# Kernel optimization log

Measured on AMD Instinct MI355X. Metric: run time of the kernel, lower is better.

Reference implementation:

```python
import jax, jax.numpy as jnp
import numpy as np
from functools import reduce

N = 20          # total qubits
N_SQC = 4       # shadow-circuit qubits
REPEAT = 2      # BasicEntangleLayer repeat
CDTYPE = jnp.complex64

_I2 = jnp.eye(2, dtype=CDTYPE)
_X  = jnp.array([[0, 1], [1, 0]], dtype=CDTYPE)   # PauliX
_P0 = jnp.array([[1, 0], [0, 0]], dtype=CDTYPE)
_P1 = jnp.array([[0, 0], [0, 1]], dtype=CDTYPE)


def multi_kron(mats):
    return reduce(jnp.kron, mats)


def _ry(t):
    c = jnp.cos(t * 0.5).astype(CDTYPE)
    s = jnp.sin(t * 0.5).astype(CDTYPE)
    return jnp.stack([jnp.stack([c, -s]), jnp.stack([s, c])])


def _rz(t):
    e = jnp.exp(-0.5j * t.astype(CDTYPE))
    z = jnp.zeros((), CDTYPE)
    return jnp.stack([jnp.stack([e, z]), jnp.stack([z, jnp.conj(e)])])


def _yzy_layer(p, n):
    # per qubit i: Ry(p[3i]) then Rz(p[3i+1]) then Ry(p[3i+2])
    mats = [_ry(p[3 * i + 2]) @ _rz(p[3 * i + 1]) @ _ry(p[3 * i]) for i in range(n)]
    return multi_kron(mats)


def _cnot(c, t, n):
    a = [_I2] * n; a[c] = _P0
    b = [_I2] * n; b[c] = _P1; b[t] = _X
    return multi_kron(a) + multi_kron(b)


def _ring_of_cnot(n):
    U = jnp.eye(2 ** n, dtype=CDTYPE)
    for i in range(n):
        U = _cnot(i, (i + 1) % n, n) @ U
    return U


def build_circuit(weight):
    """BasicEntangleLayer (YZY rotations + ring of CNOTs, repeated) + final YZYLayer."""
    n = N_SQC
    ring = _ring_of_cnot(n)
    U = jnp.eye(2 ** n, dtype=CDTYPE)
    for r in range(REPEAT):
        p = weight[3 * n * r:3 * n * (r + 1)]
        U = ring @ (_yzy_layer(p, n) @ U)
    U = _yzy_layer(weight[3 * n * REPEAT:3 * n * (REPEAT + 1)], n) @ U
    return U


def setup_inputs() -> dict:
    key = jax.random.key(0)
    k1, k2 = jax.random.split(key)
    vector_batch = jax.random.normal(k1, (32, 2 ** N), dtype=jnp.float32)
    weight = jax.random.uniform(k2, (9 * N_SQC,), dtype=jnp.float32,
                                minval=0.0, maxval=2.0 * np.pi)
    return {"vector_batch": vector_batch, "weight": weight}


def reference(vector_batch, weight):
    B = vector_batch.shape[0]
    # row-wise L2 normalization, then amplitude encoding into 2^N complex state
    norm = jnp.linalg.norm(vector_batch, axis=1, keepdims=True)
    state = (vector_batch / jnp.maximum(norm, 1e-12)).astype(CDTYPE)  # (B, 2^N)

    U = build_circuit(weight)                        # (16, 16)
    M = multi_kron([_X] * N_SQC)                     # X^{\otimes n_sqc}
    temp = U.conj().T @ M @ U                        # (16, 16) Hermitian

    d = 2 ** N_SQC
    outs = []
    for q in range(N - N_SQC + 1):
        # apply temp locally on qubits [q, q+n_sqc): identical math to
        # <state| I^{\otimes q} (x) temp (x) I^{\otimes rest} |state>
        s = state.reshape(B, 2 ** q, d, -1)          # (B, left, 16, right)
        ts = jnp.einsum('ij,bajc->baic', temp, s)
        outs.append(jnp.einsum('bajc,bajc->b', s.conj(), ts).real)
    return jnp.stack(outs, axis=1).astype(jnp.float32)  # (B, N-n_sqc+1)
```

## Files before the change

### kernel.cpp

```cpp
#include <hip/hip_runtime.h>
#include <math.h>

#define WS_TU    0
#define WS_S     256
#define WS_N     800
#define WS_PART  1024
#define WS_NPART 35840
#define WS_NEED_BYTES ((WS_NPART + 2048) * 4)

typedef _Float16 half8 __attribute__((ext_vector_type(8)));
typedef float f32x4 __attribute__((ext_vector_type(4)));

__device__ inline float2 cmul2(float2 a, float2 b) {
  return make_float2(a.x * b.x - a.y * b.y, a.x * b.y + a.y * b.x);
}

__device__ inline int ringperm(int x) {
  if ((x >> 3) & 1) x ^= 4;
  if ((x >> 2) & 1) x ^= 2;
  if ((x >> 1) & 1) x ^= 1;
  if (x & 1)        x ^= 8;
  return x;
}

__device__ inline float2 yzy_elem(const float* wgt, int layer, int r, int c) {
  float2 prod = make_float2(1.f, 0.f);
#pragma unroll
  for (int k = 0; k < 4; k++) {
    float t0 = wgt[layer * 12 + 3 * k + 0];
    float t1 = wgt[layer * 12 + 3 * k + 1];
    float t2 = wgt[layer * 12 + 3 * k + 2];
    float s0, c0, s1, c1, s2, c2;
    sincosf(0.5f * t0, &s0, &c0);
    sincosf(0.5f * t1, &s1, &c1);
    sincosf(0.5f * t2, &s2, &c2);
    float A = c2 * c0, B = s2 * s0, C = c2 * s0, D = s2 * c0;
    float2 m00 = make_float2( c1 * (A - B), -s1 * (A + B));
    float2 m01 = make_float2(-c1 * (C + D),  s1 * (C - D));
    float2 m10 = make_float2( c1 * (C + D),  s1 * (C - D));
    float2 m11 = make_float2( c1 * (A - B),  s1 * (A + B));
    int rb = (r >> (3 - k)) & 1, cb = (c >> (3 - k)) & 1;
    float2 mm = rb ? (cb ? m11 : m10) : (cb ? m01 : m00);
    prod = cmul2(prod, mm);
  }
  return prod;
}

__global__ void build_T_kernel(const float* __restrict__ wgt, float* __restrict__ ws) {
  __shared__ float2 U[256], Y[256], W[256];
  const int t = threadIdx.x;
  const int r = t >> 4, c = t & 15;

  U[t] = yzy_elem(wgt, 0, r, c);
  __syncthreads();
  W[ringperm(r) * 16 + c] = U[t];
  __syncthreads(); U[t] = W[t]; __syncthreads();
  Y[t] = yzy_elem(wgt, 1, r, c);
  __syncthreads();
  {
    float2 s = make_float2(0.f, 0.f);
#pragma unroll
    for (int k = 0; k < 16; k++) {
      float2 pr = cmul2(Y[r * 16 + k], U[k * 16 + c]);
      s.x += pr.x; s.y += pr.y;
    }
    W[t] = s;
  }
  __syncthreads(); U[t] = W[t]; __syncthreads();
  W[ringperm(r) * 16 + c] = U[t];
  __syncthreads(); U[t] = W[t]; __syncthreads();
  Y[t] = yzy_elem(wgt, 2, r, c);
  __syncthreads();
  {
    float2 s = make_float2(0.f, 0.f);
#pragma unroll
    for (int k = 0; k < 16; k++) {
      float2 pr = cmul2(Y[r * 16 + k], U[k * 16 + c]);
      s.x += pr.x; s.y += pr.y;
    }
    W[t] = s;
  }
  __syncthreads(); U[t] = W[t]; __syncthreads();
  Y[t] = U[(r ^ 15) * 16 + c];
  __syncthreads();
  float s_re = 0.f;
#pragma unroll
  for (int k = 0; k < 16; k++) {
    float2 u = U[k * 16 + r], m = Y[k * 16 + c];
    s_re += u.x * m.x + u.y * m.y;
  }
  ws[WS_TU + t] = s_re;
}

__device__ inline int swzB(int B) {
  int h = B >> 3;
  int f = (h ^ (h >> 3) ^ (h >> 6)) & 7;
  return B ^ f;
}

template <int P>
__device__ inline float windowM(const half8* __restrict__ HB, const float* __restrict__ Tr) {
  const int t = threadIdx.x;
  const int w = t >> 6, l = t & 63, g = l >> 4, i = l & 15;
  f32x4 h0 = {0.f, 0.f, 0.f, 0.f}, h1 = {0.f, 0.f, 0.f, 0.f};
#pragma unroll
  for (int s = 0; s < 4; s++) {
    int rest0 = (w << 5) | (s << 2) | g;
    int rest1 = (w << 5) | ((s + 4) << 2) | g;
    int rl0 = rest0 & ((1 << (P - 3)) - 1), rh0 = rest0 >> (P - 3);
    int rl1 = rest1 & ((1 << (P - 3)) - 1), rh1 = rest1 >> (P - 3);
    int pos0 = (rl0 << 3) | (i << P) | (rh0 << (P + 4));
    int pos1 = (rl1 << 3) | (i << P) | (rh1 << (P + 4));
    half8 f0 = HB[swzB(pos0 >> 3)];
    half8 f1 = HB[swzB(pos1 >> 3)];
    h0 = __builtin_amdgcn_mfma_f32_16x16x32_f16(f0, f0, h0, 0, 0, 0);
    h1 = __builtin_amdgcn_mfma_f32_16x16x32_f16(f1, f1, h1, 0, 0, 0);
  }
  float part = 0.f;
#pragma unroll
  for (int reg = 0; reg < 4; reg++) part = fmaf(Tr[reg], h0[reg] + h1[reg], part);
  return part;
}

__global__ __launch_bounds__(256) void passAll_kernel(const float* __restrict__ vb,
                                                      float* ws, int use_part) {
  __shared__ half8 HB[2048];
  const int t = threadIdx.x;
  const int bid = blockIdx.x;

  int mode, idx;
  if (bid < 4096) {
    int gph = bid >> 4, s = bid & 15;
    mode = s >> 3;
    idx = gph * 8 + (s & 7);
  } else {
    mode = 2;
    idx = bid - 4096;
  }
  const int b = idx >> 6, chunk = idx & 63;
  const int l = t & 63, g = l >> 4, i = l & 15;

  float Treg[4];
#pragma unroll
  for (int reg = 0; reg < 4; reg++) Treg[reg] = ws[WS_TU + ((g * 4 + reg) << 4) + i];

  float nsum = 0.f;
  if (mode == 0) {
    const float4* src4 = ((const float4*)vb) + ((size_t)b << 18) + ((size_t)chunk << 12);
#pragma unroll
    for (int j = 0; j < 8; j++) {
      int B = j * 256 + t;
      float4 a = src4[2 * B], c = src4[2 * B + 1];
      nsum = fmaf(a.x, a.x, nsum); nsum = fmaf(a.y, a.y, nsum);
      nsum = fmaf(a.z, a.z, nsum); nsum = fmaf(a.w, a.w, nsum);
      nsum = fmaf(c.x, c.x, nsum); nsum = fmaf(c.y, c.y, nsum);
      nsum = fmaf(c.z, c.z, nsum); nsum = fmaf(c.w, c.w, nsum);
      half8 h;
      h[0] = (_Float16)a.x; h[1] = (_Float16)a.y; h[2] = (_Float16)a.z; h[3] = (_Float16)a.w;
      h[4] = (_Float16)c.x; h[5] = (_Float16)c.y; h[6] = (_Float16)c.z; h[7] = (_Float16)c.w;
      HB[swzB(B)] = h;
    }
  } else if (mode == 1) {
    const float* srcf = vb + ((size_t)b << 20) + ((size_t)chunk << 14);
#pragma unroll
    for (int j = 0; j < 8; j++) {
      int B = j * 256 + t;
      half8 h;
#pragma unroll
      for (int e = 0; e < 8; e++) h[e] = (_Float16)srcf[e * 2048 + B];
      HB[swzB(B)] = h;
    }
  } else {
    const float4* src4 = ((const float4*)vb) + ((size_t)b << 18) + chunk * 8;
#pragma unroll
    for (int j = 0; j < 8; j++) {
      int B = j * 256 + t;
      int row = B >> 2;
      int c4 = (B & 3) * 2;
      float4 a = src4[row * 512 + c4], c = src4[row * 512 + c4 + 1];
      half8 h;
      h[0] = (_Float16)a.x; h[1] = (_Float16)a.y; h[2] = (_Float16)a.z; h[3] = (_Float16)a.w;
      h[4] = (_Float16)c.x; h[5] = (_Float16)c.y; h[6] = (_Float16)c.z; h[7] = (_Float16)c.w;
      HB[swzB(B)] = h;
    }
  }
  __syncthreads();

  float part[8];
#pragma unroll
  for (int k = 0; k < 8; k++) part[k] = 0.f;

  int nwin;
#define DOWIN(P, WIN) part[WIN] = windowM<P>(HB, Treg);
  if (mode == 0) {
    nwin = 8;
    DOWIN(3, 0) DOWIN(4, 1) DOWIN(5, 2) DOWIN(6, 3)
    DOWIN(7, 4) DOWIN(8, 5) DOWIN(9, 6) DOWIN(10, 7)
  } else if (mode == 1) {
    nwin = 3;
    DOWIN(3, 0) DOWIN(4, 1) DOWIN(5, 2)
  } else {
    nwin = 6;
    DOWIN(5, 0) DOWIN(6, 1) DOWIN(7, 2)
    DOWIN(8, 3) DOWIN(9, 4) DOWIN(10, 5)
  }
#undef DOWIN
  __syncthreads();

  float* red2 = (float*)HB;
#pragma unroll
  for (int k = 0; k < 8; k++) red2[k * 256 + t] = part[k];
  red2[8 * 256 + t] = nsum;
  __syncthreads();

  const int win = t >> 5, idx32 = t & 31;
  const float4* r4 = (const float4*)red2;
  float4 q0 = r4[win * 64 + idx32], q1 = r4[win * 64 + 32 + idx32];
  float s1 = (q0.x + q0.y + q0.z + q0.w) + (q1.x + q1.y + q1.z + q1.w);
#pragma unroll
  for (int off = 16; off; off >>= 1) s1 += __shfl_down(s1, off, 32);

  float s2 = 0.f;
  if (mode == 0 && win == 0) {
    float4 n0 = r4[8 * 64 + idx32], n1 = r4[8 * 64 + 32 + idx32];
    s2 = (n0.x + n0.y + n0.z + n0.w) + (n1.x + n1.y + n1.z + n1.w);
#pragma unroll
    for (int off = 16; off; off >>= 1) s2 += __shfl_down(s2, off, 32);
  }

  const int qbase = (mode == 0) ? 13 : (mode == 1) ? 16 : 5;
  if (idx32 == 0 && win < nwin) {
    int q = qbase - win;
    if (use_part) ws[WS_PART + (b * 17 + q) * 64 + chunk] = s1;
    else          atomicAdd(ws + WS_S + b * 17 + q, s1);
  }
  if (mode == 0 && t == 0) {
    if (use_part) ws[WS_NPART + b * 64 + chunk] = s2;
    else          atomicAdd(ws + WS_N + b, s2);
  }
}

__global__ void finalize_kernel(const float* __restrict__ ws, float* __restrict__ out,
                                int use_part) {
  int i = blockIdx.x * 256 + threadIdx.x;
  if (i < 544) {
    int b = i / 17;
    float s, n;
    if (use_part) {
      const float* sp = ws + WS_PART + i * 64;
      s = 0.f;
#pragma unroll 8
      for (int c = 0; c < 64; c++) s += sp[c];
      const float* np = ws + WS_NPART + b * 64;
      n = 0.f;
#pragma unroll 8
      for (int c = 0; c < 64; c++) n += np[c];
    } else {
      s = ws[WS_S + i];
      n = ws[WS_N + b];
    }
    out[i] = s / fmaxf(n, 1e-24f);
  }
}

extern "C" void kernel_launch(void* const* d_in, const int* in_sizes, int n_in,
                              void* d_out, int out_size, void* d_ws, size_t ws_size,
                              hipStream_t stream) {
  const float* vb  = (const float*)d_in[0];
  const float* wgt = (const float*)d_in[1];
  float* out = (float*)d_out;
  float* ws  = (float*)d_ws;
  int use_part = (ws_size >= (size_t)WS_NEED_BYTES) ? 1 : 0;

  hipMemsetAsync(d_ws, 0, 4096, stream);
  build_T_kernel<<<1, 256, 0, stream>>>(wgt, ws);
  passAll_kernel<<<6144, 256, 0, stream>>>(vb, ws, use_part);
  finalize_kernel<<<3, 256, 0, stream>>>(ws, out, use_part);
}
```

Baseline: 68.80 us.

## Fuse high-qubit windows into mode-0 blocks via in-register transpose

Drops the separate mode-1 blocks, which re-read the input with strided scalar loads to build the layout needed for qubit windows 14-16. Mode-0 blocks now keep their converted half8 values in registers, transpose them into shared memory after the first eight windows, and evaluate those three windows themselves. This removes one third of the blocks and their global reads. The cost is longer mode-0 blocks with extra register pressure, two more barriers, and a reworked reduction over twelve 16-lane groups.

```diff
diff --git a/kernel.cpp b/kernel.cpp
--- a/kernel.cpp
+++ b/kernel.cpp
@@ -128,15 +128,8 @@
   const int t = threadIdx.x;
   const int bid = blockIdx.x;
 
-  int mode, idx;
-  if (bid < 4096) {
-    int gph = bid >> 4, s = bid & 15;
-    mode = s >> 3;
-    idx = gph * 8 + (s & 7);
-  } else {
-    mode = 2;
-    idx = bid - 4096;
-  }
+  const int mode = (bid < 2048) ? 0 : 2;
+  const int idx = (bid < 2048) ? bid : bid - 2048;
   const int b = idx >> 6, chunk = idx & 63;
   const int l = t & 63, g = l >> 4, i = l & 15;
 
@@ -145,6 +138,7 @@
   for (int reg = 0; reg < 4; reg++) Treg[reg] = ws[WS_TU + ((g * 4 + reg) << 4) + i];
 
   float nsum = 0.f;
+  half8 h[8];
   if (mode == 0) {
     const float4* src4 = ((const float4*)vb) + ((size_t)b << 18) + ((size_t)chunk << 12);
 #pragma unroll
@@ -155,20 +149,11 @@
       nsum = fmaf(a.z, a.z, nsum); nsum = fmaf(a.w, a.w, nsum);
       nsum = fmaf(c.x, c.x, nsum); nsum = fmaf(c.y, c.y, nsum);
       nsum = fmaf(c.z, c.z, nsum); nsum = fmaf(c.w, c.w, nsum);
-      half8 h;
-      h[0] = (_Float16)a.x; h[1] = (_Float16)a.y; h[2] = (_Float16)a.z; h[3] = (_Float16)a.w;
-      h[4] = (_Float16)c.x; h[5] = (_Float16)c.y; h[6] = (_Float16)c.z; h[7] = (_Float16)c.w;
-      HB[swzB(B)] = h;
-    }
-  } else if (mode == 1) {
-    const float* srcf = vb + ((size_t)b << 20) + ((size_t)chunk << 14);
-#pragma unroll
-    for (int j = 0; j < 8; j++) {
-      int B = j * 256 + t;
-      half8 h;
-#pragma unroll
-      for (int e = 0; e < 8; e++) h[e] = (_Float16)srcf[e * 2048 + B];
-      HB[swzB(B)] = h;
+      half8 hh;
+      hh[0] = (_Float16)a.x; hh[1] = (_Float16)a.y; hh[2] = (_Float16)a.z; hh[3] = (_Float16)a.w;
+      hh[4] = (_Float16)c.x; hh[5] = (_Float16)c.y; hh[6] = (_Float16)c.z; hh[7] = (_Float16)c.w;
+      h[j] = hh;
+      HB[swzB(B)] = hh;
     }
   } else {
     const float4* src4 = ((const float4*)vb) + ((size_t)b << 18) + chunk * 8;
@@ -178,27 +163,34 @@
       int row = B >> 2;
       int c4 = (B & 3) * 2;
       float4 a = src4[row * 512 + c4], c = src4[row * 512 + c4 + 1];
-      half8 h;
-      h[0] = (_Float16)a.x; h[1] = (_Float16)a.y; h[2] = (_Float16)a.z; h[3] = (_Float16)a.w;
-      h[4] = (_Float16)c.x; h[5] = (_Float16)c.y; h[6] = (_Float16)c.z; h[7] = (_Float16)c.w;
-      HB[swzB(B)] = h;
-    }
-  }
-  __syncthreads();
-
-  float part[8];
-#pragma unroll
-  for (int k = 0; k < 8; k++) part[k] = 0.f;
+      half8 hh;
+      hh[0] = (_Float16)a.x; hh[1] = (_Float16)a.y; hh[2] = (_Float16)a.z; hh[3] = (_Float16)a.w;
+      hh[4] = (_Float16)c.x; hh[5] = (_Float16)c.y; hh[6] = (_Float16)c.z; hh[7] = (_Float16)c.w;
+      HB[swzB(B)] = hh;
+    }
+  }
+  __syncthreads();
+
+  float part[11];
+#pragma unroll
+  for (int k = 0; k < 11; k++) part[k] = 0.f;
 
   int nwin;
 #define DOWIN(P, WIN) part[WIN] = windowM<P>(HB, Treg);
   if (mode == 0) {
-    nwin = 8;
+    nwin = 11;
     DOWIN(3, 0) DOWIN(4, 1) DOWIN(5, 2) DOWIN(6, 3)
     DOWIN(7, 4) DOWIN(8, 5) DOWIN(9, 6) DOWIN(10, 7)
-  } else if (mode == 1) {
-    nwin = 3;
-    DOWIN(3, 0) DOWIN(4, 1) DOWIN(5, 2)
+    __syncthreads();
+#pragma unroll
+    for (int e = 0; e < 8; e++) {
+      half8 v;
+#pragma unroll
+      for (int j = 0; j < 8; j++) v[j] = h[j][e];
+      HB[swzB(8 * t + e)] = v;
+    }
+    __syncthreads();
+    DOWIN(3, 8) DOWIN(4, 9) DOWIN(5, 10)
   } else {
     nwin = 6;
     DOWIN(5, 0) DOWIN(6, 1) DOWIN(7, 2)
@@ -209,34 +201,36 @@
 
   float* red2 = (float*)HB;
 #pragma unroll
-  for (int k = 0; k < 8; k++) red2[k * 256 + t] = part[k];
-  red2[8 * 256 + t] = nsum;
-  __syncthreads();
-
-  const int win = t >> 5, idx32 = t & 31;
+  for (int k = 0; k < 11; k++) red2[k * 256 + t] = part[k];
+  red2[11 * 256 + t] = nsum;
+  __syncthreads();
+
+  const int win = t >> 4, idx16 = t & 15;
   const float4* r4 = (const float4*)red2;
-  float4 q0 = r4[win * 64 + idx32], q1 = r4[win * 64 + 32 + idx32];
-  float s1 = (q0.x + q0.y + q0.z + q0.w) + (q1.x + q1.y + q1.z + q1.w);
-#pragma unroll
-  for (int off = 16; off; off >>= 1) s1 += __shfl_down(s1, off, 32);
-
-  float s2 = 0.f;
-  if (mode == 0 && win == 0) {
-    float4 n0 = r4[8 * 64 + idx32], n1 = r4[8 * 64 + 32 + idx32];
-    s2 = (n0.x + n0.y + n0.z + n0.w) + (n1.x + n1.y + n1.z + n1.w);
-#pragma unroll
-    for (int off = 16; off; off >>= 1) s2 += __shfl_down(s2, off, 32);
-  }
-
-  const int qbase = (mode == 0) ? 13 : (mode == 1) ? 16 : 5;
-  if (idx32 == 0 && win < nwin) {
-    int q = qbase - win;
-    if (use_part) ws[WS_PART + (b * 17 + q) * 64 + chunk] = s1;
-    else          atomicAdd(ws + WS_S + b * 17 + q, s1);
-  }
-  if (mode == 0 && t == 0) {
-    if (use_part) ws[WS_NPART + b * 64 + chunk] = s2;
-    else          atomicAdd(ws + WS_N + b, s2);
+  float4 q0 = r4[win * 64 + idx16],      q1 = r4[win * 64 + 16 + idx16];
+  float4 q2 = r4[win * 64 + 32 + idx16], q3 = r4[win * 64 + 48 + idx16];
+  float s1 = ((q0.x + q0.y) + (q0.z + q0.w)) + ((q1.x + q1.y) + (q1.z + q1.w)) +
+             ((q2.x + q2.y) + (q2.z + q2.w)) + ((q3.x + q3.y) + (q3.z + q3.w));
+#pragma unroll
+  for (int off = 8; off; off >>= 1) s1 += __shfl_down(s1, off, 16);
+
+  if (idx16 == 0) {
+    if (mode == 0) {
+      if (win < 11) {
+        int q = (win < 8) ? (13 - win) : (24 - win);
+        if (use_part) ws[WS_PART + (b * 17 + q) * 64 + chunk] = s1;
+        else          atomicAdd(ws + WS_S + b * 17 + q, s1);
+      } else if (win == 11) {
+        if (use_part) ws[WS_NPART + b * 64 + chunk] = s1;
+        else          atomicAdd(ws + WS_N + b, s1);
+      }
+    } else {
+      if (win < 6) {
+        int q = 5 - win;
+        if (use_part) ws[WS_PART + (b * 17 + q) * 64 + chunk] = s1;
+        else          atomicAdd(ws + WS_S + b * 17 + q, s1);
+      }
+    }
   }
 }
 
@@ -274,6 +268,6 @@
 
   hipMemsetAsync(d_ws, 0, 4096, stream);
   build_T_kernel<<<1, 256, 0, stream>>>(wgt, ws);
-  passAll_kernel<<<6144, 256, 0, stream>>>(vb, ws, use_part);
+  passAll_kernel<<<4096, 256, 0, stream>>>(vb, ws, use_part);
   finalize_kernel<<<3, 256, 0, stream>>>(ws, out, use_part);
 }
```

After: 63.96 us. 1.08x faster.
